# Performance work log

Measured on AMD Instinct MI355X. Metric: run time of the kernel, lower is better.

The kernel has to match this reference:

```python
import jax, jax.numpy as jnp
import numpy as np

B, S, E, H, HD, RD, MP = 2, 2048, 1024, 16, 64, 32, 8  # batch, seq, embed, heads, head_dim, rotary_dim, mp_num


def rotate_every_two(x):
    # x: [..., D] -> interleave (-x_odd, x_even)
    x1 = x[..., ::2]
    x2 = x[..., 1::2]
    return jnp.stack((-x2, x1), axis=-1).reshape(x.shape)


def apply_rotary(x, sin, cos):
    # x: [B,S,H,RD]; sin/cos: [S, RD//2] -> repeat_interleave(2) -> [1,S,1,RD]
    sin = jnp.repeat(sin, 2, axis=-1)[None, :, None, :]
    cos = jnp.repeat(cos, 2, axis=-1)[None, :, None, :]
    return x * cos + rotate_every_two(x) * sin


def setup_inputs() -> dict:
    key = jax.random.key(0)
    k1, k2, k3 = jax.random.split(key, 3)
    return {
        "hidden_states": jax.random.normal(k1, (B, S, E), dtype=jnp.float32),
        "w_qkv": jax.random.normal(k2, (3 * E, E), dtype=jnp.float32) * 0.02,
        "w_out": jax.random.normal(k3, (E, E), dtype=jnp.float32) * 0.02,
    }


def reference(hidden_states, w_qkv, w_out):
    qkv = hidden_states @ w_qkv.T                      # [B,S,3E]
    local = HD * H // MP                               # 128
    qkv = qkv.reshape(B, S, MP, 3 * local)
    # torch.split order in source is (query, value, key)
    q, v, k = jnp.split(qkv, 3, axis=-1)               # each [B,S,MP,local]

    def split_heads(x):
        return x.reshape(B, S, MP, H // MP, HD).reshape(B, S, H, HD)

    q, k, v = split_heads(q), split_heads(k), split_heads(v)  # [B,S,H,HD]

    # fixed sinusoidal rotary embedding over first RD dims
    inv_freq = 1.0 / 10000 ** (jnp.arange(0, RD, 2, dtype=jnp.float32) / RD)
    sinusoid = jnp.arange(S, dtype=jnp.float32)[:, None] * inv_freq[None, :]  # [S, RD//2]
    sin, cos = jnp.sin(sinusoid), jnp.cos(sinusoid)

    q = jnp.concatenate([apply_rotary(q[..., :RD], sin, cos), q[..., RD:]], axis=-1)
    k = jnp.concatenate([apply_rotary(k[..., :RD], sin, cos), k[..., RD:]], axis=-1)

    # [B,H,S,HD]
    q = q.transpose(0, 2, 1, 3)
    k = k.transpose(0, 2, 1, 3)
    v = v.transpose(0, 2, 1, 3)

    scores = jnp.einsum('bhqd,bhkd->bhqk', q, k) / np.float32(np.sqrt(HD))
    causal = jnp.tril(jnp.ones((S, S), dtype=bool))
    scores = jnp.where(causal[None, None], scores, jnp.float32(-1e9))
    attn = jax.nn.softmax(scores.astype(jnp.float32), axis=-1).astype(q.dtype)
    out = jnp.einsum('bhqk,bhkd->bhqd', attn, v)       # [B,H,S,HD]
    out = out.transpose(0, 2, 1, 3).reshape(B, S, E)
    return out @ w_out.T
```

## Files before the change

### kernel.cpp

```cpp
#include <hip/hip_runtime.h>
#include <hip/hip_bf16.h>

typedef __attribute__((ext_vector_type(8))) short short8;
typedef __attribute__((ext_vector_type(4))) float v4f;

#define ASYNC_COPY16(ldsptr, gptr)                                                        \
  __builtin_amdgcn_global_load_lds((const __attribute__((address_space(1))) void*)(gptr), \
                                   (__attribute__((address_space(3))) void*)(ldsptr),     \
                                   16, 0, 0)

__device__ __forceinline__ unsigned short f2bf(float f) {
  unsigned int u = __float_as_uint(f);
  u += 0x7fffu + ((u >> 16) & 1u);
  return (unsigned short)(u >> 16);
}
__device__ __forceinline__ float bf2f(unsigned short s) {
  return __uint_as_float(((unsigned int)s) << 16);
}

__global__ void convert_all(const float* __restrict__ h, const float* __restrict__ wq,
                            const float* __restrict__ wo, unsigned short* __restrict__ ho,
                            unsigned short* __restrict__ wqo, unsigned short* __restrict__ woo) {
  int i = (blockIdx.x * blockDim.x + threadIdx.x) * 4;
  const float* src;
  unsigned short* dst;
  int j;
  if (i < 4194304) { src = h; dst = ho; j = i; }
  else if (i < 7340032) { src = wq; dst = wqo; j = i - 4194304; }
  else { src = wo; dst = woo; j = i - 7340032; }
  float4 v = *(const float4*)(src + j);
  ushort4 o;
  o.x = f2bf(v.x); o.y = f2bf(v.y); o.z = f2bf(v.z); o.w = f2bf(v.w);
  *(ushort4*)(dst + j) = o;
}

template <int BN, bool BF16OUT>
__global__ __launch_bounds__(256) void gemm_bt(const unsigned short* __restrict__ A,
                                               const unsigned short* __restrict__ Bm,
                                               void* __restrict__ Cv, int M, int N, int K) {
  constexpr int WN = BN / 2;
  constexpr int JN = WN / 16;
  __shared__ __attribute__((aligned(16))) unsigned short As[128 * 32];
  __shared__ __attribute__((aligned(16))) unsigned short Bs[BN * 32];
  int t = threadIdx.x;
  int w = t >> 6, lane = t & 63, kb = lane >> 4, lr = lane & 15;
  int m0 = blockIdx.y * 128, n0 = blockIdx.x * BN;
  int wm = (w >> 1) * 64, wn = (w & 1) * WN;
  v4f acc[4][JN];
#pragma unroll
  for (int i = 0; i < 4; i++)
#pragma unroll
    for (int j = 0; j < JN; j++) acc[i][j] = (v4f){0.f, 0.f, 0.f, 0.f};
  int ra = m0 + (t >> 2);
  int rb = n0 + (t >> 2);
  int ca = (t & 3) * 8;
  for (int k0 = 0; k0 < K; k0 += 32) {
    ASYNC_COPY16(&As[t * 8],        A + (size_t)ra * K + k0 + ca);
    ASYNC_COPY16(&As[2048 + t * 8], A + (size_t)(ra + 64) * K + k0 + ca);
#pragma unroll
    for (int c = 0; c < BN / 64; c++)
      ASYNC_COPY16(&Bs[c * 2048 + t * 8], Bm + (size_t)(rb + c * 64) * K + k0 + ca);
    __syncthreads();
    short8 av[4], bv[JN];
#pragma unroll
    for (int i = 0; i < 4; i++) av[i] = *(const short8*)&As[(wm + i * 16 + lr) * 32 + kb * 8];
#pragma unroll
    for (int j = 0; j < JN; j++) bv[j] = *(const short8*)&Bs[(wn + j * 16 + lr) * 32 + kb * 8];
#pragma unroll
    for (int i = 0; i < 4; i++)
#pragma unroll
      for (int j = 0; j < JN; j++)
        acc[i][j] = __builtin_amdgcn_mfma_f32_16x16x32_bf16(av[i], bv[j], acc[i][j], 0, 0, 0);
    __syncthreads();
  }
#pragma unroll
  for (int i = 0; i < 4; i++) {
    int row = m0 + wm + i * 16 + kb * 4;
#pragma unroll
    for (int j = 0; j < JN; j++) {
      int col = n0 + wn + j * 16 + lr;
#pragma unroll
      for (int r = 0; r < 4; r++) {
        if (BF16OUT)
          ((unsigned short*)Cv)[(size_t)(row + r) * N + col] = f2bf(acc[i][j][r]);
        else
          ((float*)Cv)[(size_t)(row + r) * N + col] = acc[i][j][r];
      }
    }
  }
}

__global__ __launch_bounds__(256) void rope_vt(const unsigned short* __restrict__ qkv,
                                               unsigned short* __restrict__ Q,
                                               unsigned short* __restrict__ Ko,
                                               unsigned short* __restrict__ Vt) {
  __shared__ float tile[64][65];
  int t = threadIdx.x;
  int bh = blockIdx.y, s0 = blockIdx.x * 64;
  int b = bh >> 4, h = bh & 15;
  int mp = h >> 1, ii = h & 1;
  int hbase = mp * 384 + ii * 64;
  int tx = t & 63, ty = t >> 6;
#pragma unroll
  for (int q16 = 0; q16 < 16; q16++) {
    int srow = q16 * 4 + ty;
    tile[srow][tx] = bf2f(qkv[(size_t)(b * 2048 + s0 + srow) * 3072 + hbase + 128 + tx]);
  }
  int sl = t >> 2, ch = t & 3;
  int s = s0 + sl;
  size_t ib = (size_t)(b * 2048 + s) * 3072 + hbase + ch * 16;
  short8 qv0 = *(const short8*)(qkv + ib);
  short8 qv1 = *(const short8*)(qkv + ib + 8);
  short8 kv0 = *(const short8*)(qkv + ib + 256);
  short8 kv1 = *(const short8*)(qkv + ib + 264);
  float qf[16], kf[16];
#pragma unroll
  for (int j = 0; j < 8; j++) {
    qf[j] = bf2f((unsigned short)qv0[j]); qf[8 + j] = bf2f((unsigned short)qv1[j]);
    kf[j] = bf2f((unsigned short)kv0[j]); kf[8 + j] = bf2f((unsigned short)kv1[j]);
  }
  if (ch < 2) {
#pragma unroll
    for (int jj = 0; jj < 8; jj++) {
      int j = ch * 8 + jj;
      float ang = (float)s * expf(-(float)j * 0.57564627324851142f);
      float sn, cs;
      sincosf(ang, &sn, &cs);
      float a = qf[2 * jj], bq = qf[2 * jj + 1];
      qf[2 * jj] = a * cs - bq * sn; qf[2 * jj + 1] = bq * cs + a * sn;
      float c2 = kf[2 * jj], d2 = kf[2 * jj + 1];
      kf[2 * jj] = c2 * cs - d2 * sn; kf[2 * jj + 1] = d2 * cs + c2 * sn;
    }
  }
  const float qs = 0.125f * 1.4426950408889634f;
  unsigned short qo[16], ko[16];
#pragma unroll
  for (int j = 0; j < 16; j++) { qo[j] = f2bf(qs * qf[j]); ko[j] = f2bf(kf[j]); }
  size_t ob = (size_t)(bh * 2048 + s) * 64 + ch * 16;
  *(short8*)(Q + ob) = *(short8*)qo;
  *(short8*)(Q + ob + 8) = *(short8*)(qo + 8);
  *(short8*)(Ko + ob) = *(short8*)ko;
  *(short8*)(Ko + ob + 8) = *(short8*)(ko + 8);
  __syncthreads();
#pragma unroll
  for (int q16 = 0; q16 < 16; q16++) {
    int drow = q16 * 4 + ty;
    int p = ((tx & 15) * 2 + ((tx >> 4) & 1)) | (tx & 32);
    Vt[(size_t)bh * 64 * 2048 + (size_t)drow * 2048 + s0 + p] = f2bf(tile[tx][drow]);
  }
}

__global__ __launch_bounds__(256, 6) void attn_fused(const unsigned short* __restrict__ Qg,
                                                     const unsigned short* __restrict__ Kg,
                                                     const unsigned short* __restrict__ Vtg,
                                                     unsigned short* __restrict__ AO) {
  __shared__ __attribute__((aligned(16))) unsigned short Ks[2 * 2048];
  __shared__ __attribute__((aligned(16))) unsigned short Vs[2 * 2048];
  __shared__ __attribute__((aligned(16))) unsigned short Ps[4 * 16 * 40];
  int t = threadIdx.x;
  int w = t >> 6, lane = t & 63, kb = lane >> 4, lr = lane & 15;
  int gid = blockIdx.x;
  int z = gid & 7;
  int bh = (gid >> 3) & 31;
  int quarter = gid >> 8;
  int qtile = (quarter == 0) ? z : (quarter == 1) ? (31 - z) : (quarter == 2) ? (z + 8) : (23 - z);
  int m0 = qtile * 64;
  const unsigned short* Qb = Qg + (size_t)bh * 2048 * 64;
  const unsigned short* Kb = Kg + (size_t)bh * 2048 * 64;
  const unsigned short* Vb = Vtg + (size_t)bh * 64 * 2048;

  short8 aq0 = *(const short8*)(Qb + (size_t)(m0 + w * 16 + lr) * 64 + kb * 8);
  short8 aq1 = *(const short8*)(Qb + (size_t)(m0 + w * 16 + lr) * 64 + 32 + kb * 8);

  v4f acc[4];
  float lp[4];
#pragma unroll
  for (int n = 0; n < 4; n++) acc[n] = (v4f){0.f, 0.f, 0.f, 0.f};
#pragma unroll
  for (int r = 0; r < 4; r++) lp[r] = 0.f;

  int nkt = 2 * qtile + 2;
  int mrow = w * 16 + kb * 4;

  int kc = t >> 5, krow_s = t & 31;
  int vc = t >> 6, vd = t & 63;
  auto stage = [&](int kt, int buf) {
    int base = buf * 2048;
    ASYNC_COPY16(&Ks[base + t * 8], Kb + (size_t)(kt * 32 + krow_s) * 64 + kc * 8);
    ASYNC_COPY16(&Vs[base + t * 8], Vb + (size_t)vd * 2048 + kt * 32 + vc * 8);
  };

  stage(0, 0);
  __syncthreads();

  unsigned short* Pw = &Ps[w * 640];
  for (int kt = 0; kt < nkt; kt++) {
    int cur = (kt & 1) * 2048;
    if (kt + 1 < nkt) stage(kt + 1, (kt + 1) & 1);
    v4f sc[2];
#pragma unroll
    for (int n2 = 0; n2 < 2; n2++) {
      int krow = n2 * 16 + lr;
      short8 bk0 = *(const short8*)&Ks[cur + (kb * 32 + krow) * 8];
      short8 bk1 = *(const short8*)&Ks[cur + ((kb + 4) * 32 + krow) * 8];
      v4f zz = (v4f){0.f, 0.f, 0.f, 0.f};
      zz = __builtin_amdgcn_mfma_f32_16x16x32_bf16(aq0, bk0, zz, 0, 0, 0);
      zz = __builtin_amdgcn_mfma_f32_16x16x32_bf16(aq1, bk1, zz, 0, 0, 0);
      sc[n2] = zz;
    }
    if (kt >= 2 * qtile) {
#pragma unroll
      for (int n2 = 0; n2 < 2; n2++)
#pragma unroll
        for (int r = 0; r < 4; r++) {
          int key = kt * 32 + n2 * 16 + lr;
          if (key > m0 + mrow + r) sc[n2][r] = -1e30f;
        }
    }
#pragma unroll
    for (int r = 0; r < 4; r++) {
      float p0 = exp2f(sc[0][r]);
      float p1 = exp2f(sc[1][r]);
      lp[r] += p0 + p1;
      __hip_bfloat162 pb = __float22bfloat162_rn(float2{p0, p1});
      *(__hip_bfloat162*)&Pw[(mrow & 15) * 40 + r * 40 + lr * 2] = pb;
    }
    short8 ap = *(const short8*)&Pw[lr * 40 + kb * 8];
#pragma unroll
    for (int dt = 0; dt < 4; dt++) {
      int d = dt * 16 + lr;
      short8 bv = *(const short8*)&Vs[cur + (kb * 64 + d) * 8];
      acc[dt] = __builtin_amdgcn_mfma_f32_16x16x32_bf16(ap, bv, acc[dt], 0, 0, 0);
    }
    __syncthreads();
  }
  int b = bh >> 4, h = bh & 15;
#pragma unroll
  for (int r = 0; r < 4; r++) {
    float s = lp[r];
#pragma unroll
    for (int off = 1; off < 16; off <<= 1) s += __shfl_xor(s, off);
    float inv = 1.0f / s;
    int qrow = m0 + mrow + r;
#pragma unroll
    for (int dt = 0; dt < 4; dt++)
      AO[(size_t)(b * 2048 + qrow) * 1024 + h * 64 + dt * 16 + lr] = f2bf(acc[dt][r] * inv);
  }
}

extern "C" void kernel_launch(void* const* d_in, const int* in_sizes, int n_in,
                              void* d_out, int out_size, void* d_ws, size_t ws_size,
                              hipStream_t stream) {
  const float* hidden = (const float*)d_in[0];
  const float* w_qkv = (const float*)d_in[1];
  const float* w_out = (const float*)d_in[2];
  float* out = (float*)d_out;
  char* ws = (char*)d_ws;
  unsigned short* hid_bf = (unsigned short*)(ws);
  unsigned short* wqkv_bf = (unsigned short*)(ws + (8ull << 20));
  unsigned short* wout_bf = (unsigned short*)(ws + (14ull << 20));
  unsigned short* qkv_bf = (unsigned short*)(ws + (16ull << 20));
  unsigned short* Qb = (unsigned short*)(ws + (40ull << 20));
  unsigned short* Kb = (unsigned short*)(ws + (48ull << 20));
  unsigned short* Vt = (unsigned short*)(ws + (56ull << 20));
  unsigned short* AO = (unsigned short*)(ws + (64ull << 20));

  convert_all<<<8192, 256, 0, stream>>>(hidden, w_qkv, w_out, hid_bf, wqkv_bf, wout_bf);
  gemm_bt<128, true><<<dim3(24, 32), 256, 0, stream>>>(hid_bf, wqkv_bf, qkv_bf, 4096, 3072, 1024);
  rope_vt<<<dim3(32, 32), 256, 0, stream>>>(qkv_bf, Qb, Kb, Vt);
  attn_fused<<<1024, 256, 0, stream>>>(Qb, Kb, Vt, AO);
  gemm_bt<64, false><<<dim3(16, 32), 256, 0, stream>>>(AO, wout_bf, out, 4096, 1024, 1024);
}
```

Measured before the change: 207.0 us.

## Fuse RoPE, Q scaling and V transpose into the QKV GEMM epilogue

The separate rope_vt kernel is removed. The QKV GEMM epilogue now applies rotary embedding through lane shuffles, scales Q, and writes Q/K in head-major layout and V transposed directly. This avoids a round trip of the bf16 qkv buffer through global memory and one kernel launch. The cost is scattered, poorly coalesced epilogue stores (V transposed per element) and sincos work inside the GEMM. The attention block-to-(bh,qtile) mapping is also remapped, likely for cache locality.

```diff
diff --git a/kernel.cpp b/kernel.cpp
--- a/kernel.cpp
+++ b/kernel.cpp
@@ -13,9 +13,6 @@
   unsigned int u = __float_as_uint(f);
   u += 0x7fffu + ((u >> 16) & 1u);
   return (unsigned short)(u >> 16);
-}
-__device__ __forceinline__ float bf2f(unsigned short s) {
-  return __uint_as_float(((unsigned int)s) << 16);
 }
 
 __global__ void convert_all(const float* __restrict__ h, const float* __restrict__ wq,
@@ -34,10 +31,10 @@
   *(ushort4*)(dst + j) = o;
 }
 
-template <int BN, bool BF16OUT>
+template <int BN>
 __global__ __launch_bounds__(256) void gemm_bt(const unsigned short* __restrict__ A,
                                                const unsigned short* __restrict__ Bm,
-                                               void* __restrict__ Cv, int M, int N, int K) {
+                                               float* __restrict__ C, int M, int N, int K) {
   constexpr int WN = BN / 2;
   constexpr int JN = WN / 16;
   __shared__ __attribute__((aligned(16))) unsigned short As[128 * 32];
@@ -80,73 +77,107 @@
     for (int j = 0; j < JN; j++) {
       int col = n0 + wn + j * 16 + lr;
 #pragma unroll
-      for (int r = 0; r < 4; r++) {
-        if (BF16OUT)
-          ((unsigned short*)Cv)[(size_t)(row + r) * N + col] = f2bf(acc[i][j][r]);
-        else
-          ((float*)Cv)[(size_t)(row + r) * N + col] = acc[i][j][r];
+      for (int r = 0; r < 4; r++) C[(size_t)(row + r) * N + col] = acc[i][j][r];
+    }
+  }
+}
+
+__global__ __launch_bounds__(256) void gemm_qkv(const unsigned short* __restrict__ A,
+                                                const unsigned short* __restrict__ Bm,
+                                                unsigned short* __restrict__ Q,
+                                                unsigned short* __restrict__ Ko,
+                                                unsigned short* __restrict__ Vt) {
+  constexpr int Kd = 1024;
+  __shared__ __attribute__((aligned(16))) unsigned short As[128 * 32];
+  __shared__ __attribute__((aligned(16))) unsigned short Bs[128 * 32];
+  int t = threadIdx.x;
+  int w = t >> 6, lane = t & 63, kb = lane >> 4, lr = lane & 15;
+  int m0 = blockIdx.y * 128, n0 = blockIdx.x * 128;
+  int wm = (w >> 1) * 64, wn = (w & 1) * 64;
+  v4f acc[4][4];
+#pragma unroll
+  for (int i = 0; i < 4; i++)
+#pragma unroll
+    for (int j = 0; j < 4; j++) acc[i][j] = (v4f){0.f, 0.f, 0.f, 0.f};
+  int ra = m0 + (t >> 2);
+  int rb = n0 + (t >> 2);
+  int ca = (t & 3) * 8;
+  for (int k0 = 0; k0 < Kd; k0 += 32) {
+    ASYNC_COPY16(&As[t * 8],        A + (size_t)ra * Kd + k0 + ca);
+    ASYNC_COPY16(&As[2048 + t * 8], A + (size_t)(ra + 64) * Kd + k0 + ca);
+    ASYNC_COPY16(&Bs[t * 8],        Bm + (size_t)rb * Kd + k0 + ca);
+    ASYNC_COPY16(&Bs[2048 + t * 8], Bm + (size_t)(rb + 64) * Kd + k0 + ca);
+    __syncthreads();
+    short8 av[4], bv[4];
+#pragma unroll
+    for (int i = 0; i < 4; i++) av[i] = *(const short8*)&As[(wm + i * 16 + lr) * 32 + kb * 8];
+#pragma unroll
+    for (int j = 0; j < 4; j++) bv[j] = *(const short8*)&Bs[(wn + j * 16 + lr) * 32 + kb * 8];
+#pragma unroll
+    for (int i = 0; i < 4; i++)
+#pragma unroll
+      for (int j = 0; j < 4; j++)
+        acc[i][j] = __builtin_amdgcn_mfma_f32_16x16x32_bf16(av[i], bv[j], acc[i][j], 0, 0, 0);
+    __syncthreads();
+  }
+  int X = n0 >> 7;
+  int mp = X / 3;
+  int type = X - mp * 3;
+  int ii = wn >> 6;
+  int h = mp * 2 + ii;
+  const float qs = 0.125f * 1.4426950408889634f;
+  if (type == 1) {
+#pragma unroll
+    for (int i = 0; i < 4; i++) {
+      int row = m0 + wm + i * 16 + kb * 4;
+#pragma unroll
+      for (int j = 0; j < 4; j++) {
+        int dim = j * 16 + lr;
+#pragma unroll
+        for (int r = 0; r < 4; r++) {
+          int m = row + r;
+          int b = m >> 11, sl = m & 2047;
+          int bh = b * 16 + h;
+          int p = (sl & ~31) | ((sl & 15) << 1) | ((sl >> 4) & 1);
+          Vt[(size_t)bh * 131072 + (size_t)dim * 2048 + p] = f2bf(acc[i][j][r]);
+        }
       }
     }
-  }
-}
-
-__global__ __launch_bounds__(256) void rope_vt(const unsigned short* __restrict__ qkv,
-                                               unsigned short* __restrict__ Q,
-                                               unsigned short* __restrict__ Ko,
-                                               unsigned short* __restrict__ Vt) {
-  __shared__ float tile[64][65];
-  int t = threadIdx.x;
-  int bh = blockIdx.y, s0 = blockIdx.x * 64;
-  int b = bh >> 4, h = bh & 15;
-  int mp = h >> 1, ii = h & 1;
-  int hbase = mp * 384 + ii * 64;
-  int tx = t & 63, ty = t >> 6;
-#pragma unroll
-  for (int q16 = 0; q16 < 16; q16++) {
-    int srow = q16 * 4 + ty;
-    tile[srow][tx] = bf2f(qkv[(size_t)(b * 2048 + s0 + srow) * 3072 + hbase + 128 + tx]);
-  }
-  int sl = t >> 2, ch = t & 3;
-  int s = s0 + sl;
-  size_t ib = (size_t)(b * 2048 + s) * 3072 + hbase + ch * 16;
-  short8 qv0 = *(const short8*)(qkv + ib);
-  short8 qv1 = *(const short8*)(qkv + ib + 8);
-  short8 kv0 = *(const short8*)(qkv + ib + 256);
-  short8 kv1 = *(const short8*)(qkv + ib + 264);
-  float qf[16], kf[16];
-#pragma unroll
-  for (int j = 0; j < 8; j++) {
-    qf[j] = bf2f((unsigned short)qv0[j]); qf[8 + j] = bf2f((unsigned short)qv1[j]);
-    kf[j] = bf2f((unsigned short)kv0[j]); kf[8 + j] = bf2f((unsigned short)kv1[j]);
-  }
-  if (ch < 2) {
-#pragma unroll
-    for (int jj = 0; jj < 8; jj++) {
-      int j = ch * 8 + jj;
-      float ang = (float)s * expf(-(float)j * 0.57564627324851142f);
-      float sn, cs;
-      sincosf(ang, &sn, &cs);
-      float a = qf[2 * jj], bq = qf[2 * jj + 1];
-      qf[2 * jj] = a * cs - bq * sn; qf[2 * jj + 1] = bq * cs + a * sn;
-      float c2 = kf[2 * jj], d2 = kf[2 * jj + 1];
-      kf[2 * jj] = c2 * cs - d2 * sn; kf[2 * jj + 1] = d2 * cs + c2 * sn;
-    }
-  }
-  const float qs = 0.125f * 1.4426950408889634f;
-  unsigned short qo[16], ko[16];
-#pragma unroll
-  for (int j = 0; j < 16; j++) { qo[j] = f2bf(qs * qf[j]); ko[j] = f2bf(kf[j]); }
-  size_t ob = (size_t)(bh * 2048 + s) * 64 + ch * 16;
-  *(short8*)(Q + ob) = *(short8*)qo;
-  *(short8*)(Q + ob + 8) = *(short8*)(qo + 8);
-  *(short8*)(Ko + ob) = *(short8*)ko;
-  *(short8*)(Ko + ob + 8) = *(short8*)(ko + 8);
-  __syncthreads();
-#pragma unroll
-  for (int q16 = 0; q16 < 16; q16++) {
-    int drow = q16 * 4 + ty;
-    int p = ((tx & 15) * 2 + ((tx >> 4) & 1)) | (tx & 32);
-    Vt[(size_t)bh * 64 * 2048 + (size_t)drow * 2048 + s0 + p] = f2bf(tile[tx][drow]);
+  } else {
+    unsigned short* dst = (type == 0) ? Q : Ko;
+    float scale = (type == 0) ? qs : 1.0f;
+#pragma unroll
+    for (int i = 0; i < 4; i++) {
+      int row = m0 + wm + i * 16 + kb * 4;
+#pragma unroll
+      for (int j = 0; j < 4; j++) {
+        int dim = j * 16 + lr;
+        float vals[4];
+#pragma unroll
+        for (int r = 0; r < 4; r++) vals[r] = acc[i][j][r];
+        if (j < 2) {
+          int jp = dim >> 1;
+          float invf = expf(-(float)jp * 0.57564627324851142f);
+#pragma unroll
+          for (int r = 0; r < 4; r++) {
+            int sl = (row + r) & 2047;
+            float ang = (float)sl * invf;
+            float sn, cs;
+            sincosf(ang, &sn, &cs);
+            float partner = __shfl_xor(vals[r], 1);
+            float self = vals[r] * cs;
+            vals[r] = (lr & 1) ? fmaf(partner, sn, self) : fmaf(-partner, sn, self);
+          }
+        }
+#pragma unroll
+        for (int r = 0; r < 4; r++) {
+          int m = row + r;
+          int b = m >> 11, sl = m & 2047;
+          int bh = b * 16 + h;
+          dst[(((size_t)(bh * 2048 + sl)) << 6) + dim] = f2bf(vals[r] * scale);
+        }
+      }
+    }
   }
 }
 
@@ -160,9 +191,11 @@
   int t = threadIdx.x;
   int w = t >> 6, lane = t & 63, kb = lane >> 4, lr = lane & 15;
   int gid = blockIdx.x;
-  int z = gid & 7;
-  int bh = (gid >> 3) & 31;
+  int g3 = gid & 7;
+  int b2 = (gid >> 3) & 3;
+  int z = (gid >> 5) & 7;
   int quarter = gid >> 8;
+  int bh = g3 * 4 + b2;
   int qtile = (quarter == 0) ? z : (quarter == 1) ? (31 - z) : (quarter == 2) ? (z + 8) : (23 - z);
   int m0 = qtile * 64;
   const unsigned short* Qb = Qg + (size_t)bh * 2048 * 64;
@@ -259,15 +292,13 @@
   unsigned short* hid_bf = (unsigned short*)(ws);
   unsigned short* wqkv_bf = (unsigned short*)(ws + (8ull << 20));
   unsigned short* wout_bf = (unsigned short*)(ws + (14ull << 20));
-  unsigned short* qkv_bf = (unsigned short*)(ws + (16ull << 20));
-  unsigned short* Qb = (unsigned short*)(ws + (40ull << 20));
-  unsigned short* Kb = (unsigned short*)(ws + (48ull << 20));
-  unsigned short* Vt = (unsigned short*)(ws + (56ull << 20));
-  unsigned short* AO = (unsigned short*)(ws + (64ull << 20));
+  unsigned short* Qb = (unsigned short*)(ws + (16ull << 20));
+  unsigned short* Kb = (unsigned short*)(ws + (24ull << 20));
+  unsigned short* Vt = (unsigned short*)(ws + (32ull << 20));
+  unsigned short* AO = (unsigned short*)(ws + (40ull << 20));
 
   convert_all<<<8192, 256, 0, stream>>>(hidden, w_qkv, w_out, hid_bf, wqkv_bf, wout_bf);
-  gemm_bt<128, true><<<dim3(24, 32), 256, 0, stream>>>(hid_bf, wqkv_bf, qkv_bf, 4096, 3072, 1024);
-  rope_vt<<<dim3(32, 32), 256, 0, stream>>>(qkv_bf, Qb, Kb, Vt);
+  gemm_qkv<<<dim3(24, 32), 256, 0, stream>>>(hid_bf, wqkv_bf, Qb, Kb, Vt);
   attn_fused<<<1024, 256, 0, stream>>>(Qb, Kb, Vt, AO);
-  gemm_bt<64, false><<<dim3(16, 32), 256, 0, stream>>>(AO, wout_bf, out, 4096, 1024, 1024);
-}
+  gemm_bt<64><<<dim3(16, 32), 256, 0, stream>>>(AO, wout_bf, out, 4096, 1024, 1024);
+}
```

Measured after the change: 207.8 us. About the same (+0.4%).
